# Performance work log

Measured on AMD Instinct MI355X. Metric: run time of the kernel, lower is better.

## Reference

```python
import jax, jax.numpy as jnp
import numpy as np

D_MODEL = 128
D_STATE = 256
D_CONV = 4
EXPAND = 2
D_INNER = EXPAND * D_MODEL  # 256 == D_STATE (required by the module's einsum/add)
B = 4
L = 100  # fixed: self.C has first dim 100


def silu(x):
    return x * jax.nn.sigmoid(x)


def setup_inputs() -> dict:
    key = jax.random.key(0)
    ks = jax.random.split(key, 10)
    s = 0.02
    dt_std = D_INNER ** (-0.5)
    inp = {
        "hidden_states": jax.random.normal(ks[0], (B, L, D_MODEL), jnp.float32),
        "state": jax.random.normal(ks[1], (B, L, D_INNER, D_STATE), jnp.float32),
        # torch nn.Linear layout: (out_features, in_features)
        "in_proj_w": jax.random.normal(ks[2], (2 * D_INNER, D_MODEL), jnp.float32) * s,
        "in_proj_b": jnp.zeros((2 * D_INNER,), jnp.float32),
        # depthwise conv1d weight: (d_inner, 1, d_conv)
        "conv_w": jax.random.normal(ks[3], (D_INNER, 1, D_CONV), jnp.float32) * s,
        "conv_b": jnp.zeros((D_INNER,), jnp.float32),
        "x_proj_w": jax.random.normal(ks[4], (2 * D_STATE, D_INNER), jnp.float32) * s,
        "dt_proj_w": jax.random.uniform(ks[5], (D_INNER, D_INNER), jnp.float32, -dt_std, dt_std),
        "dt_proj_b": jnp.zeros((D_INNER,), jnp.float32),
        # A_log = log(arange(1, d_state+1)) broadcast to (d_inner, d_state)
        "A_log": jnp.log(jnp.broadcast_to(jnp.arange(1, D_STATE + 1, dtype=jnp.float32), (D_INNER, D_STATE))),
        "D1": jnp.ones((D_INNER,), jnp.float32),
        # torch inits self.C to ones; add tiny noise to avoid degenerate baseline
        "C_param": jnp.ones((L, D_STATE, D_STATE), jnp.float32) + jax.random.normal(ks[6], (L, D_STATE, D_STATE), jnp.float32) * 0.01,
        "out_proj_w": jax.random.normal(ks[7], (D_MODEL, D_INNER), jnp.float32) * s,
        "out_proj_b": jnp.zeros((D_MODEL,), jnp.float32),
    }
    return inp


def reference(hidden_states, state, in_proj_w, in_proj_b, conv_w, conv_b,
              x_proj_w, dt_proj_w, dt_proj_b, A_log, D1, C_param,
              out_proj_w, out_proj_b):
    b, l, _ = hidden_states.shape
    xz = hidden_states @ in_proj_w.T + in_proj_b          # (b, l, 2*d_inner)
    x, z = jnp.split(xz, 2, axis=-1)                      # each (b, l, d_inner)

    # causal depthwise conv: pad (d_conv-1) left == conv with pad both sides then [:, :, :l]
    xc = jnp.transpose(x, (0, 2, 1))                      # (b, d_inner, l)
    xc = jax.lax.conv_general_dilated(
        xc, conv_w, window_strides=(1,), padding=[(conv_w.shape[-1] - 1, 0)],
        dimension_numbers=("NCH", "OIH", "NCH"), feature_group_count=xc.shape[1])
    xc = xc + conv_b[None, :, None]
    x = silu(jnp.transpose(xc, (0, 2, 1)))                # (b, l, d_inner)

    bc = x @ x_proj_w.T                                   # (b, l, 2*d_state)
    Bm, _Cm_unused = jnp.split(bc, 2, axis=-1)            # torch shadows chunked C with self.C

    dt = jax.nn.softplus(x @ dt_proj_w.T + dt_proj_b)     # (b, l, d_inner)
    A = -jnp.exp(A_log)                                   # (d_inner, d_state)
    dA = jnp.exp(dt[..., None] * A)                       # (b, l, d_inner, d_state)
    dB = dt[..., None] * Bm[..., None, :]                 # (b, l, d_inner, d_state)
    actual_state = state * dA + dB                        # elementwise 'blnd,blnd->blnd'

    y = jnp.einsum("bldn,ldn->bln", actual_state, C_param) + D1 * x  # (b, l, d_inner)
    y = y * silu(z)
    out = y @ out_proj_w.T + out_proj_b                   # (b, l, d_model)
    return out, actual_state
```

## Files before the change

### kernel.cpp

```cpp
#include <hip/hip_runtime.h>

#define D_MODEL 128
#define D_INNER 256
#define D_STATE 256
#define LEN 100
#define NR 400

__device__ __forceinline__ float siluf_(float x) { return x / (1.0f + __expf(-x)); }
__device__ __forceinline__ float softplusf_(float x) {
    return (x > 20.f) ? x : log1pf(expf(x));
}

__global__ void k_inproj(const float* __restrict__ hidden, const float* __restrict__ w,
                         const float* __restrict__ b, float* __restrict__ xz) {
    int idx = blockIdx.x * 256 + threadIdx.x;
    int r = idx >> 9, j = idx & 511;
    const float* hp = hidden + r * D_MODEL;
    const float* wp = w + j * D_MODEL;
    float acc = 0.f;
#pragma unroll
    for (int k = 0; k < D_MODEL; k += 4) {
        float4 a = *reinterpret_cast<const float4*>(hp + k);
        float4 c = *reinterpret_cast<const float4*>(wp + k);
        acc += a.x * c.x + a.y * c.y + a.z * c.z + a.w * c.w;
    }
    xz[idx] = acc + b[j];
}

__global__ void k_nega(const float* __restrict__ alog, float* __restrict__ negA) {
    int i = blockIdx.x * 256 + threadIdx.x;
    negA[i] = -expf(alog[i]);
}

__global__ void k_conv(const float* __restrict__ xz, const float* __restrict__ cw,
                       const float* __restrict__ cb, float* __restrict__ xact) {
    int idx = blockIdx.x * 256 + threadIdx.x;
    int r = idx >> 8, c = idx & 255;
    int l = r % LEN;
    float4 w = *reinterpret_cast<const float4*>(cw + c * 4);
    float acc = cb[c];
    if (l >= 3) acc += xz[(r - 3) * 512 + c] * w.x;
    if (l >= 2) acc += xz[(r - 2) * 512 + c] * w.y;
    if (l >= 1) acc += xz[(r - 1) * 512 + c] * w.z;
    acc += xz[r * 512 + c] * w.w;
    xact[idx] = siluf_(acc);
}

__global__ void k_bdt(const float* __restrict__ xact, const float* __restrict__ xw,
                      const float* __restrict__ dtw, const float* __restrict__ dtb,
                      float* __restrict__ Bm, float* __restrict__ dt) {
    int idx = blockIdx.x * 256 + threadIdx.x;
    int r = idx >> 9, j = idx & 511;
    bool isB = (j < 256);
    int jj = isB ? j : (j - 256);
    const float* xp = xact + r * 256;
    const float* wp = (isB ? xw : dtw) + jj * 256;
    float acc = 0.f;
#pragma unroll 4
    for (int k = 0; k < 256; k += 4) {
        float4 a = *reinterpret_cast<const float4*>(xp + k);
        float4 c = *reinterpret_cast<const float4*>(wp + k);
        acc += a.x * c.x + a.y * c.y + a.z * c.z + a.w * c.w;
    }
    if (isB) Bm[r * 256 + jj] = acc;
    else     dt[r * 256 + jj] = softplusf_(acc + dtb[jj]);
}

__global__ void k_scan(const float* __restrict__ state, const float* __restrict__ negA,
                       const float* __restrict__ Cp, const float* __restrict__ dt,
                       const float* __restrict__ Bm, float* __restrict__ ostate,
                       float* __restrict__ ypart) {
    int bid = blockIdx.x;
    int r = bid >> 3, sl = bid & 7, d0 = sl * 32;
    int l = r % LEN;
    int t = threadIdx.x;
    int n0 = t * 4;
    __shared__ float dts[32];
    if (t < 32) dts[t] = dt[r * 256 + d0 + t];
    __syncthreads();
    float4 Bv = *reinterpret_cast<const float4*>(Bm + r * 256 + n0);
    const float* sp = state + ((size_t)(r * 256 + d0)) * 256 + n0;
    const float* cp = Cp + ((size_t)(l * 256 + d0)) * 256 + n0;
    const float* ap = negA + d0 * 256 + n0;
    float* op = ostate + ((size_t)(r * 256 + d0)) * 256 + n0;
    float4 acc = make_float4(0.f, 0.f, 0.f, 0.f);
#pragma unroll 4
    for (int dd = 0; dd < 32; ++dd) {
        float dtv = dts[dd];
        float4 s = *reinterpret_cast<const float4*>(sp + (size_t)dd * 256);
        float4 c = *reinterpret_cast<const float4*>(cp + (size_t)dd * 256);
        float4 a = *reinterpret_cast<const float4*>(ap + dd * 256);
        float4 as;
        as.x = s.x * __expf(dtv * a.x) + dtv * Bv.x;
        as.y = s.y * __expf(dtv * a.y) + dtv * Bv.y;
        as.z = s.z * __expf(dtv * a.z) + dtv * Bv.z;
        as.w = s.w * __expf(dtv * a.w) + dtv * Bv.w;
        *reinterpret_cast<float4*>(op + (size_t)dd * 256) = as;
        acc.x += as.x * c.x;
        acc.y += as.y * c.y;
        acc.z += as.z * c.z;
        acc.w += as.w * c.w;
    }
    *reinterpret_cast<float4*>(ypart + ((size_t)(sl * NR + r)) * 256 + n0) = acc;
}

__global__ void k_yfin(const float* __restrict__ ypart, const float* __restrict__ xact,
                       const float* __restrict__ xz, const float* __restrict__ D1,
                       float* __restrict__ y) {
    int idx = blockIdx.x * 256 + threadIdx.x;
    int r = idx >> 8, n = idx & 255;
    const int S = NR * 256;
    float s = 0.f;
#pragma unroll
    for (int q = 0; q < 8; q++) s += ypart[q * S + idx];
    s += D1[n] * xact[idx];
    y[idx] = s * siluf_(xz[r * 512 + 256 + n]);
}

__global__ void k_outproj(const float* __restrict__ y, const float* __restrict__ ow,
                          const float* __restrict__ ob, float* __restrict__ out) {
    int idx = blockIdx.x * 256 + threadIdx.x;
    int r = idx >> 7, m = idx & 127;
    const float* yp = y + r * 256;
    const float* wp = ow + m * 256;
    float acc = ob[m];
#pragma unroll 4
    for (int k = 0; k < 256; k += 4) {
        float4 a = *reinterpret_cast<const float4*>(yp + k);
        float4 c = *reinterpret_cast<const float4*>(wp + k);
        acc += a.x * c.x + a.y * c.y + a.z * c.z + a.w * c.w;
    }
    out[idx] = acc;
}

extern "C" void kernel_launch(void* const* d_in, const int* in_sizes, int n_in,
                              void* d_out, int out_size, void* d_ws, size_t ws_size,
                              hipStream_t stream) {
    const float* hidden = (const float*)d_in[0];
    const float* state  = (const float*)d_in[1];
    const float* ipw    = (const float*)d_in[2];
    const float* ipb    = (const float*)d_in[3];
    const float* cw     = (const float*)d_in[4];
    const float* cb     = (const float*)d_in[5];
    const float* xpw    = (const float*)d_in[6];
    const float* dtw    = (const float*)d_in[7];
    const float* dtb    = (const float*)d_in[8];
    const float* alog   = (const float*)d_in[9];
    const float* D1     = (const float*)d_in[10];
    const float* Cp     = (const float*)d_in[11];
    const float* opw    = (const float*)d_in[12];
    const float* opb    = (const float*)d_in[13];

    float* out    = (float*)d_out;
    float* ostate = out + 51200;

    float* ws    = (float*)d_ws;
    float* xz    = ws;
    float* xact  = ws + 204800;
    float* Bm    = ws + 307200;
    float* dt    = ws + 409600;
    float* negA  = ws + 512000;
    float* ypart = ws + 577536;
    float* y     = ws + 1396736;

    k_inproj <<<800, 256, 0, stream>>>(hidden, ipw, ipb, xz);
    k_nega   <<<256, 256, 0, stream>>>(alog, negA);
    k_conv   <<<400, 256, 0, stream>>>(xz, cw, cb, xact);
    k_bdt    <<<800, 256, 0, stream>>>(xact, xpw, dtw, dtb, Bm, dt);
    k_scan   <<<3200, 64, 0, stream>>>(state, negA, Cp, dt, Bm, ostate, ypart);
    k_yfin   <<<400, 256, 0, stream>>>(ypart, xact, xz, D1, y);
    k_outproj<<<200, 256, 0, stream>>>(y, opw, opb, out);
}
```

Before: 317.8 us.

## Fuse front and back stages into per-row kernels and widen scan blocks

Merges in_proj, the causal conv, the x_proj/dt_proj GEMVs and silu(z) into a single per-row kernel. Each block recomputes the x projection for the three previous rows so the xz buffer round trip goes away. Merges the y combination and out_proj into one kernel, and changes the scan to 256-thread blocks that reduce four wavefronts' partial sums in shared memory, which cuts the partial-sum buffer from 8 slices to 4. Launch count drops from 7 to 4, in exchange for redundant in_proj work and fewer, heavier front blocks.

New measurement: 297.3 us. 1.07x faster.

```diff
diff --git a/kernel.cpp b/kernel.cpp
--- a/kernel.cpp
+++ b/kernel.cpp
@@ -1,8 +1,5 @@
 #include <hip/hip_runtime.h>
 
-#define D_MODEL 128
-#define D_INNER 256
-#define D_STATE 256
 #define LEN 100
 #define NR 400
 
@@ -11,126 +8,156 @@
     return (x > 20.f) ? x : log1pf(expf(x));
 }
 
-__global__ void k_inproj(const float* __restrict__ hidden, const float* __restrict__ w,
-                         const float* __restrict__ b, float* __restrict__ xz) {
-    int idx = blockIdx.x * 256 + threadIdx.x;
-    int r = idx >> 9, j = idx & 511;
-    const float* hp = hidden + r * D_MODEL;
-    const float* wp = w + j * D_MODEL;
-    float acc = 0.f;
-#pragma unroll
-    for (int k = 0; k < D_MODEL; k += 4) {
-        float4 a = *reinterpret_cast<const float4*>(hp + k);
-        float4 c = *reinterpret_cast<const float4*>(wp + k);
-        acc += a.x * c.x + a.y * c.y + a.z * c.z + a.w * c.w;
-    }
-    xz[idx] = acc + b[j];
-}
-
 __global__ void k_nega(const float* __restrict__ alog, float* __restrict__ negA) {
     int i = blockIdx.x * 256 + threadIdx.x;
     negA[i] = -expf(alog[i]);
 }
 
-__global__ void k_conv(const float* __restrict__ xz, const float* __restrict__ cw,
-                       const float* __restrict__ cb, float* __restrict__ xact) {
-    int idx = blockIdx.x * 256 + threadIdx.x;
-    int r = idx >> 8, c = idx & 255;
+__global__ void __launch_bounds__(256) k_front(
+    const float* __restrict__ hidden, const float* __restrict__ ipw, const float* __restrict__ ipb,
+    const float* __restrict__ cw, const float* __restrict__ cb,
+    const float* __restrict__ xpw, const float* __restrict__ dtw, const float* __restrict__ dtb,
+    float* __restrict__ xact, float* __restrict__ Bm, float* __restrict__ dt,
+    float* __restrict__ zs)
+{
+    int r = blockIdx.x;
     int l = r % LEN;
-    float4 w = *reinterpret_cast<const float4*>(cw + c * 4);
-    float acc = cb[c];
-    if (l >= 3) acc += xz[(r - 3) * 512 + c] * w.x;
-    if (l >= 2) acc += xz[(r - 2) * 512 + c] * w.y;
-    if (l >= 1) acc += xz[(r - 1) * 512 + c] * w.z;
-    acc += xz[r * 512 + c] * w.w;
-    xact[idx] = siluf_(acc);
+    int j = threadIdx.x;
+    int lb = l < 3 ? l : 3;
+    __shared__ float hid[4][128];
+    __shared__ __align__(16) float xs[256];
+
+    for (int e = j; e < 512; e += 256) {
+        int k = e >> 7;
+        int c = e & 127;
+        hid[k][c]       = (k     <= lb) ? hidden[(size_t)(r - k)     * 128 + c] : 0.f;
+        hid[k + 2][c]   = 0.f;
+        if (k + 2 <= lb) hid[k + 2][c] = hidden[(size_t)(r - k - 2) * 128 + c];
+    }
+    __syncthreads();
+
+    float b0 = ipb[j];
+    float xp0 = b0, xp1 = b0, xp2 = b0, xp3 = b0;
+    float z = ipb[256 + j];
+    const float* wx = ipw + (size_t)j * 128;
+    const float* wz = ipw + (size_t)(256 + j) * 128;
+#pragma unroll 8
+    for (int c = 0; c < 128; c += 4) {
+        float4 w = *(const float4*)(wx + c);
+        xp0 += w.x * hid[0][c] + w.y * hid[0][c+1] + w.z * hid[0][c+2] + w.w * hid[0][c+3];
+        xp1 += w.x * hid[1][c] + w.y * hid[1][c+1] + w.z * hid[1][c+2] + w.w * hid[1][c+3];
+        xp2 += w.x * hid[2][c] + w.y * hid[2][c+1] + w.z * hid[2][c+2] + w.w * hid[2][c+3];
+        xp3 += w.x * hid[3][c] + w.y * hid[3][c+1] + w.z * hid[3][c+2] + w.w * hid[3][c+3];
+        float4 v = *(const float4*)(wz + c);
+        z += v.x * hid[0][c] + v.y * hid[0][c+1] + v.z * hid[0][c+2] + v.w * hid[0][c+3];
+    }
+    float4 w4 = *(const float4*)(cw + j * 4);
+    float conv = cb[j] + w4.w * xp0;
+    if (lb >= 1) conv += w4.z * xp1;
+    if (lb >= 2) conv += w4.y * xp2;
+    if (lb >= 3) conv += w4.x * xp3;
+    float xa = siluf_(conv);
+    xs[j] = xa;
+    xact[r * 256 + j] = xa;
+    zs[r * 256 + j] = siluf_(z);
+    __syncthreads();
+
+    float accB = 0.f, accD = dtb[j];
+    const float* bw = xpw + (size_t)j * 256;
+    const float* dw = dtw + (size_t)j * 256;
+#pragma unroll 8
+    for (int c = 0; c < 256; c += 4) {
+        float4 bwv = *(const float4*)(bw + c);
+        float4 dwv = *(const float4*)(dw + c);
+        float4 xv  = *(const float4*)(xs + c);
+        accB += bwv.x * xv.x + bwv.y * xv.y + bwv.z * xv.z + bwv.w * xv.w;
+        accD += dwv.x * xv.x + dwv.y * xv.y + dwv.z * xv.z + dwv.w * xv.w;
+    }
+    Bm[r * 256 + j] = accB;
+    dt[r * 256 + j] = softplusf_(accD);
 }
 
-__global__ void k_bdt(const float* __restrict__ xact, const float* __restrict__ xw,
-                      const float* __restrict__ dtw, const float* __restrict__ dtb,
-                      float* __restrict__ Bm, float* __restrict__ dt) {
-    int idx = blockIdx.x * 256 + threadIdx.x;
-    int r = idx >> 9, j = idx & 511;
-    bool isB = (j < 256);
-    int jj = isB ? j : (j - 256);
-    const float* xp = xact + r * 256;
-    const float* wp = (isB ? xw : dtw) + jj * 256;
-    float acc = 0.f;
-#pragma unroll 4
-    for (int k = 0; k < 256; k += 4) {
-        float4 a = *reinterpret_cast<const float4*>(xp + k);
-        float4 c = *reinterpret_cast<const float4*>(wp + k);
-        acc += a.x * c.x + a.y * c.y + a.z * c.z + a.w * c.w;
-    }
-    if (isB) Bm[r * 256 + jj] = acc;
-    else     dt[r * 256 + jj] = softplusf_(acc + dtb[jj]);
-}
-
-__global__ void k_scan(const float* __restrict__ state, const float* __restrict__ negA,
-                       const float* __restrict__ Cp, const float* __restrict__ dt,
-                       const float* __restrict__ Bm, float* __restrict__ ostate,
-                       float* __restrict__ ypart) {
+__global__ void __launch_bounds__(256) k_scan(
+    const float* __restrict__ state, const float* __restrict__ negA,
+    const float* __restrict__ Cp, const float* __restrict__ dt,
+    const float* __restrict__ Bm, float* __restrict__ ostate, float* __restrict__ ypart)
+{
     int bid = blockIdx.x;
-    int r = bid >> 3, sl = bid & 7, d0 = sl * 32;
+    int r = bid >> 2, ch = bid & 3;
     int l = r % LEN;
-    int t = threadIdx.x;
-    int n0 = t * 4;
-    __shared__ float dts[32];
-    if (t < 32) dts[t] = dt[r * 256 + d0 + t];
+    int tid = threadIdx.x;
+    int wid = tid >> 6, lane = tid & 63, n0 = lane * 4;
+    int d0 = ch * 64 + wid * 16;
+    __shared__ float dts[64];
+    __shared__ __align__(16) float accs[4][256];
+    if (tid < 64) dts[tid] = dt[r * 256 + ch * 64 + tid];
     __syncthreads();
-    float4 Bv = *reinterpret_cast<const float4*>(Bm + r * 256 + n0);
+    float4 Bv = *(const float4*)(Bm + r * 256 + n0);
     const float* sp = state + ((size_t)(r * 256 + d0)) * 256 + n0;
     const float* cp = Cp + ((size_t)(l * 256 + d0)) * 256 + n0;
-    const float* ap = negA + d0 * 256 + n0;
+    const float* ap = negA + (size_t)d0 * 256 + n0;
     float* op = ostate + ((size_t)(r * 256 + d0)) * 256 + n0;
     float4 acc = make_float4(0.f, 0.f, 0.f, 0.f);
 #pragma unroll 4
-    for (int dd = 0; dd < 32; ++dd) {
-        float dtv = dts[dd];
-        float4 s = *reinterpret_cast<const float4*>(sp + (size_t)dd * 256);
-        float4 c = *reinterpret_cast<const float4*>(cp + (size_t)dd * 256);
-        float4 a = *reinterpret_cast<const float4*>(ap + dd * 256);
+    for (int i = 0; i < 16; ++i) {
+        float dtv = dts[wid * 16 + i];
+        float4 s = *(const float4*)(sp + (size_t)i * 256);
+        float4 c = *(const float4*)(cp + (size_t)i * 256);
+        float4 a = *(const float4*)(ap + (size_t)i * 256);
         float4 as;
         as.x = s.x * __expf(dtv * a.x) + dtv * Bv.x;
         as.y = s.y * __expf(dtv * a.y) + dtv * Bv.y;
         as.z = s.z * __expf(dtv * a.z) + dtv * Bv.z;
         as.w = s.w * __expf(dtv * a.w) + dtv * Bv.w;
-        *reinterpret_cast<float4*>(op + (size_t)dd * 256) = as;
+        *(float4*)(op + (size_t)i * 256) = as;
         acc.x += as.x * c.x;
         acc.y += as.y * c.y;
         acc.z += as.z * c.z;
         acc.w += as.w * c.w;
     }
-    *reinterpret_cast<float4*>(ypart + ((size_t)(sl * NR + r)) * 256 + n0) = acc;
+    *(float4*)(&accs[wid][n0]) = acc;
+    __syncthreads();
+    if (wid == 0) {
+        float4 t0 = *(const float4*)(&accs[0][n0]);
+        float4 t1 = *(const float4*)(&accs[1][n0]);
+        float4 t2 = *(const float4*)(&accs[2][n0]);
+        float4 t3 = *(const float4*)(&accs[3][n0]);
+        float4 o;
+        o.x = t0.x + t1.x + t2.x + t3.x;
+        o.y = t0.y + t1.y + t2.y + t3.y;
+        o.z = t0.z + t1.z + t2.z + t3.z;
+        o.w = t0.w + t1.w + t2.w + t3.w;
+        *(float4*)(ypart + ((size_t)(ch * NR + r)) * 256 + n0) = o;
+    }
 }
 
-__global__ void k_yfin(const float* __restrict__ ypart, const float* __restrict__ xact,
-                       const float* __restrict__ xz, const float* __restrict__ D1,
-                       float* __restrict__ y) {
-    int idx = blockIdx.x * 256 + threadIdx.x;
-    int r = idx >> 8, n = idx & 255;
+__global__ void __launch_bounds__(256) k_back(
+    const float* __restrict__ ypart, const float* __restrict__ xact,
+    const float* __restrict__ zs, const float* __restrict__ D1,
+    const float* __restrict__ ow, const float* __restrict__ ob,
+    float* __restrict__ out)
+{
+    int r = blockIdx.x;
+    int t = threadIdx.x;
+    __shared__ __align__(16) float ys[256];
     const int S = NR * 256;
-    float s = 0.f;
-#pragma unroll
-    for (int q = 0; q < 8; q++) s += ypart[q * S + idx];
-    s += D1[n] * xact[idx];
-    y[idx] = s * siluf_(xz[r * 512 + 256 + n]);
-}
-
-__global__ void k_outproj(const float* __restrict__ y, const float* __restrict__ ow,
-                          const float* __restrict__ ob, float* __restrict__ out) {
-    int idx = blockIdx.x * 256 + threadIdx.x;
-    int r = idx >> 7, m = idx & 127;
-    const float* yp = y + r * 256;
-    const float* wp = ow + m * 256;
-    float acc = ob[m];
-#pragma unroll 4
-    for (int k = 0; k < 256; k += 4) {
-        float4 a = *reinterpret_cast<const float4*>(yp + k);
-        float4 c = *reinterpret_cast<const float4*>(wp + k);
-        acc += a.x * c.x + a.y * c.y + a.z * c.z + a.w * c.w;
+    int idx = r * 256 + t;
+    float v = ypart[idx] + ypart[S + idx] + ypart[2 * S + idx] + ypart[3 * S + idx];
+    v += D1[t] * xact[idx];
+    v *= zs[idx];
+    ys[t] = v;
+    __syncthreads();
+    if (t < 128) {
+        const float* wp = ow + (size_t)t * 256;
+        float acc = ob[t];
+#pragma unroll 8
+        for (int c = 0; c < 256; c += 4) {
+            float4 w = *(const float4*)(wp + c);
+            float4 x = *(const float4*)(ys + c);
+            acc += w.x * x.x + w.y * x.y + w.z * x.z + w.w * x.w;
+        }
+        out[r * 128 + t] = acc;
     }
-    out[idx] = acc;
 }
 
 extern "C" void kernel_launch(void* const* d_in, const int* in_sizes, int n_in,
@@ -155,19 +182,16 @@
     float* ostate = out + 51200;
 
     float* ws    = (float*)d_ws;
-    float* xz    = ws;
-    float* xact  = ws + 204800;
-    float* Bm    = ws + 307200;
-    float* dt    = ws + 409600;
-    float* negA  = ws + 512000;
-    float* ypart = ws + 577536;
-    float* y     = ws + 1396736;
+    float* negA  = ws;
+    float* xact  = ws + 65536;
+    float* Bm    = ws + 167936;
+    float* dt    = ws + 270336;
+    float* zs    = ws + 372736;
+    float* ypart = ws + 475136;
 
-    k_inproj <<<800, 256, 0, stream>>>(hidden, ipw, ipb, xz);
-    k_nega   <<<256, 256, 0, stream>>>(alog, negA);
-    k_conv   <<<400, 256, 0, stream>>>(xz, cw, cb, xact);
-    k_bdt    <<<800, 256, 0, stream>>>(xact, xpw, dtw, dtb, Bm, dt);
-    k_scan   <<<3200, 64, 0, stream>>>(state, negA, Cp, dt, Bm, ostate, ypart);
-    k_yfin   <<<400, 256, 0, stream>>>(ypart, xact, xz, D1, y);
-    k_outproj<<<200, 256, 0, stream>>>(y, opw, opb, out);
+    k_nega <<<256,  256, 0, stream>>>(alog, negA);
+    k_front<<<400,  256, 0, stream>>>(hidden, ipw, ipb, cw, cb, xpw, dtw, dtb,
+                                      xact, Bm, dt, zs);
+    k_scan <<<1600, 256, 0, stream>>>(state, negA, Cp, dt, Bm, ostate, ypart);
+    k_back <<<400,  256, 0, stream>>>(ypart, xact, zs, D1, opw, opb, out);
 }
```
